# Kernel tuning notes

Hardware: AMD Instinct MI355X
Metric: run time of the kernel (lower is better)

The kernel has to match this reference:

```python
import jax, jax.numpy as jnp
import numpy as np

B, C_IN, C_OUT, D, H, W = 2, 128, 128, 16, 32, 32


def setup_inputs() -> dict:
    key = jax.random.key(0)
    kx, kw, kb = jax.random.split(key, 3)
    x = jax.random.normal(kx, (B, C_IN, D, H, W), dtype=jnp.float32)
    # ddpm_conv3x3 -> Conv3d(in_ch, out_ch, kernel=3, padding=1) with default (scaled-variance) init
    fan_in = C_IN * 3 * 3 * 3
    scale = 1.0 / np.sqrt(fan_in)
    Wk = jax.random.uniform(kw, (C_OUT, C_IN, 3, 3, 3), dtype=jnp.float32, minval=-scale, maxval=scale)
    b = jnp.zeros((C_OUT,), dtype=jnp.float32)
    return {"x": x, "Wk": Wk, "b": b}


def reference(x, Wk, b):
    h = jnp.repeat(jnp.repeat(jnp.repeat(x, 2, axis=2), 2, axis=3), 2, axis=4)
    # 3x3x3 conv, stride 1, padding 1 (SAME)
    out = jax.lax.conv_general_dilated(
        h, Wk,
        window_strides=(1, 1, 1),
        padding="SAME",
        dimension_numbers=("NCDHW", "OIDHW", "NCDHW"),
    )
    return out + b[None, :, None, None, None]
```

## Files before the change

kernel.cpp:

```cpp
#include <hip/hip_runtime.h>
#include <hip/hip_bf16.h>

#define B_    2
#define CIN   128
#define COUT  128
#define DD    16
#define HH    32
#define WW    32
#define OS_H2 64
#define OS_D2 (64*64)
#define OS_CO (32*64*64)
#define OS_B  (COUT*OS_CO)

#define PD_D   18
#define PD_H   34
#define RD     17
#define RDB    68
#define HWDW   (PD_H*RD)
#define PLB    (HWDW*4)
#define CIW    (PD_D*HWDW)
#define CIB    (CIW*4)
#define CI8B   (8*CIB)
#define ARRD   ((size_t)B_*CIN*CIW)
#define ARRB   (ARRD*4)
#define AFOLD_BYTES (8*32*8*64*16)

typedef __attribute__((ext_vector_type(8))) short        short8;
typedef __attribute__((ext_vector_type(4))) float        floatx4;
typedef __attribute__((ext_vector_type(4))) unsigned int uint4v;

static __device__ __forceinline__ unsigned f2bf(float f) {
    union { __hip_bfloat16 h; unsigned short u; } cv;
    cv.h = __float2bfloat16(f);
    return (unsigned)cv.u;
}

__global__ __launch_bounds__(256) void fold_kernel(const float* __restrict__ Wk,
                                                   unsigned short* __restrict__ Afold) {
    const int t = blockIdx.x * 256 + threadIdx.x;
    const int p  = t >> 14;
    const int ks = (t >> 9) & 31;
    const int ct = (t >> 6) & 7;
    const int l  = t & 63;
    const int co = ct * 16 + (l & 15);
    const int ci = ks * 4 + (l >> 4);
    const int ed = (p >> 2) & 1, eh = (p >> 1) & 1, ew = p & 1;

    const float* w = Wk + (co * CIN + ci) * 27;
    float wv[27];
    #pragma unroll
    for (int i = 0; i < 27; ++i) wv[i] = w[i];

    short8 pk;
    #pragma unroll
    for (int tt = 0; tt < 8; ++tt) {
        const int td = (tt >> 2) & 1, th = (tt >> 1) & 1, tw = tt & 1;
        const int dlo = ed ? (td ? 2 : 0) : (td ? 1 : 0);
        const int dhi = ed ? (td ? 2 : 1) : (td ? 2 : 0);
        const int hlo = eh ? (th ? 2 : 0) : (th ? 1 : 0);
        const int hhi = eh ? (th ? 2 : 1) : (th ? 2 : 0);
        const int wlo = ew ? (tw ? 2 : 0) : (tw ? 1 : 0);
        const int whi = ew ? (tw ? 2 : 1) : (tw ? 2 : 0);
        float s = 0.f;
        for (int kd = dlo; kd <= dhi; ++kd)
            for (int kh = hlo; kh <= hhi; ++kh)
                for (int kw = wlo; kw <= whi; ++kw)
                    s += wv[kd * 9 + kh * 3 + kw];
        pk[tt] = (short)f2bf(s);
    }
    reinterpret_cast<short8*>(Afold)[t] = pk;
}

__global__ __launch_bounds__(256) void pad_kernel(const float* __restrict__ x,
                                                  unsigned* __restrict__ xe) {
    const int idx = blockIdx.x * 256 + threadIdx.x;
    const int w2 = idx & 15;
    const int h  = (idx >> 4) & 31;
    const int d  = (idx >> 9) & 15;
    const int ci = (idx >> 13) & 127;
    const int b  = (idx >> 20) & 1;
    const float2 v = *reinterpret_cast<const float2*>(
        x + (size_t)((b * CIN + ci) * DD + d) * (HH * WW) + h * WW + w2 * 2);
    xe[(size_t)((b * CIN + ci) * PD_D + d + 1) * HWDW
       + (h + 1) * RD + (w2 + 1)] = f2bf(v.x) | (f2bf(v.y) << 16);
}

__global__ __launch_bounds__(256) void xo_kernel(const unsigned* __restrict__ xe,
                                                 unsigned* __restrict__ xo) {
    const size_t t = (size_t)blockIdx.x * 256 + threadIdx.x;
    const unsigned e0 = xe[t];
    const unsigned e1 = (t + 1 < ARRD) ? xe[t + 1] : 0u;
    xo[t] = (e0 >> 16) | (e1 << 16);
}

__global__ __launch_bounds__(256, 3) void upconv_mfma(
    const char* __restrict__ xe_c, const char* __restrict__ xo_c,
    const unsigned short* __restrict__ Afold,
    const float* __restrict__ bias,
    float* __restrict__ out)
{
    __shared__ short Bt[2][128 * 64];
    char* buf0 = reinterpret_cast<char*>(&Bt[0][0]);
    char* buf1 = reinterpret_cast<char*>(&Bt[1][0]);

    const int tid  = threadIdx.x;
    const int wave = tid >> 6;
    const int lane = tid & 63;

    const int d      = blockIdx.x >> 3;
    const int h_base = (blockIdx.x & 7) * 4;
    const int p      = blockIdx.y;
    const int b      = blockIdx.z;
    const int ed = (p >> 2) & 1, eh = (p >> 1) & 1, ew = p & 1;

    const int npair = tid & 63;
    const int grp   = tid >> 6;
    const int hl    = npair >> 4;
    const int s     = npair & 15;
    const int n_a   = hl * 32 + 2 * s;
    const int n_b   = n_a + 1;
    const char* pa = ew ? xe_c : xo_c;
    const char* pb = ew ? xo_c : xe_c;
    const int dpad0 = d + ed;
    const int hpad0 = h_base + hl + eh;
    const long rowb = ((long)(b * CIN + grp * 2) * PD_D + dpad0) * (long)PLB
                    + (long)hpad0 * RDB;
    int offA[2], offB[2];
    offA[0] = (int)rowb + (s + ew) * 4;
    offB[0] = (int)rowb + (s + 1) * 4;
    offA[1] = offA[0] + CIB;
    offB[1] = offB[0] + CIB;

    int waddr_a[2], waddr_b[2];
    #pragma unroll
    for (int i = 0; i < 2; ++i) {
        const int cl = grp * 2 + i;
        waddr_a[i] = n_a * 128 + ((cl * 16) ^ (((n_a >> 1) & 7) << 4));
        waddr_b[i] = n_b * 128 + ((cl * 16) ^ (((n_b >> 1) & 7) << 4));
    }

    const int co0 = (wave >> 1) * 64;
    const int n0  = (wave & 1) * 64;
    const int ct0 = (wave >> 1) * 4;
    int raddr[2][4];
    #pragma unroll
    for (int ksl = 0; ksl < 2; ++ksl)
        #pragma unroll
        for (int nt = 0; nt < 4; ++nt) {
            const int n  = n0 + nt * 16 + (lane & 15);
            const int kb = ksl * 64 + (lane >> 4) * 16;
            raddr[ksl][nt] = n * 128 + (kb ^ (((n >> 1) & 7) << 4));
        }

    floatx4 acc[4][4];
    #pragma unroll
    for (int i = 0; i < 4; ++i)
        #pragma unroll
        for (int j = 0; j < 4; ++j)
            acc[i][j] = (floatx4){0.f, 0.f, 0.f, 0.f};

    const short8* Ap = reinterpret_cast<const short8*>(Afold);

    unsigned ga[2][4], gb[2][4];

    #define GATHER()                                                            \
        do {                                                                    \
            _Pragma("unroll")                                                   \
            for (int i = 0; i < 2; ++i) {                                       \
                const char* ba = pa + offA[i];                                  \
                const char* bb = pb + offB[i];                                  \
                ga[i][0] = *(const unsigned*)(ba + 0);                          \
                ga[i][1] = *(const unsigned*)(ba + RDB);                        \
                ga[i][2] = *(const unsigned*)(ba + PLB);                        \
                ga[i][3] = *(const unsigned*)(ba + PLB + RDB);                  \
                gb[i][0] = *(const unsigned*)(bb + 0);                          \
                gb[i][1] = *(const unsigned*)(bb + RDB);                        \
                gb[i][2] = *(const unsigned*)(bb + PLB);                        \
                gb[i][3] = *(const unsigned*)(bb + PLB + RDB);                  \
                offA[i] += CI8B; offB[i] += CI8B;                               \
            }                                                                   \
        } while (0)

    #define BODY(kc, bufc, dofill)                                              \
        do {                                                                    \
            short8 a[2][4];                                                     \
            _Pragma("unroll")                                                   \
            for (int ksl = 0; ksl < 2; ++ksl)                                   \
                _Pragma("unroll")                                               \
                for (int ct = 0; ct < 4; ++ct)                                  \
                    a[ksl][ct] = Ap[(size_t)(((p) * 32 + (kc) * 2 + ksl) * 8    \
                                             + ct0 + ct) * 64 + lane];          \
            _Pragma("unroll")                                                   \
            for (int i = 0; i < 2; ++i) {                                       \
                *(uint4v*)(bufc + waddr_a[i]) =                                 \
                    (uint4v){ga[i][0], ga[i][1], ga[i][2], ga[i][3]};           \
                *(uint4v*)(bufc + waddr_b[i]) =                                 \
                    (uint4v){gb[i][0], gb[i][1], gb[i][2], gb[i][3]};           \
            }                                                                   \
            if (dofill) GATHER();                                               \
            asm volatile("s_waitcnt lgkmcnt(0)\n\ts_barrier" ::: "memory");     \
            __builtin_amdgcn_s_setprio(1);                                      \
            _Pragma("unroll")                                                   \
            for (int ksl = 0; ksl < 2; ++ksl) {                                 \
                short8 bfr[4];                                                  \
                _Pragma("unroll")                                               \
                for (int nt = 0; nt < 4; ++nt)                                  \
                    bfr[nt] = *reinterpret_cast<const short8*>(                 \
                        (bufc) + raddr[ksl][nt]);                               \
                _Pragma("unroll")                                               \
                for (int ct = 0; ct < 4; ++ct)                                  \
                    _Pragma("unroll")                                           \
                    for (int nt = 0; nt < 4; ++nt)                              \
                        acc[ct][nt] = __builtin_amdgcn_mfma_f32_16x16x32_bf16(  \
                            a[ksl][ct], bfr[nt], acc[ct][nt], 0, 0, 0);         \
            }                                                                   \
            __builtin_amdgcn_s_setprio(0);                                      \
        } while (0)

    GATHER();
    for (int kc = 0; kc < 16; kc += 2) {
        BODY(kc,     buf0, true);
        BODY(kc + 1, buf1, (kc + 1) != 15);
    }
    #undef BODY
    #undef GATHER

    float* ob = out + (size_t)b * OS_B + (size_t)(2 * d + ed) * OS_D2;
    #pragma unroll
    for (int ct = 0; ct < 4; ++ct) {
        #pragma unroll
        for (int j = 0; j < 4; ++j) {
            const int co = co0 + ct * 16 + (lane >> 4) * 4 + j;
            const float bv = bias[co];
            #pragma unroll
            for (int nt = 0; nt < 4; ++nt) {
                const int n  = n0 + nt * 16 + (lane & 15);
                const int hh = n >> 5, wl = n & 31;
                const int h2 = 2 * (h_base + hh) + eh;
                const int w2 = 2 * wl + ew;
                ob[(size_t)co * OS_CO + h2 * OS_H2 + w2] = acc[ct][nt][j] + bv;
            }
        }
    }
}

extern "C" void kernel_launch(void* const* d_in, const int* in_sizes, int n_in,
                              void* d_out, int out_size, void* d_ws, size_t ws_size,
                              hipStream_t stream) {
    const float* x    = (const float*)d_in[0];
    const float* Wk   = (const float*)d_in[1];
    const float* bias = (const float*)d_in[2];
    float* out        = (float*)d_out;

    unsigned short* Afold = (unsigned short*)d_ws;
    char* xe = (char*)d_ws + AFOLD_BYTES;
    char* xo = xe + ARRB;

    hipMemsetAsync(xe, 0, ARRB, stream);
    pad_kernel<<<8192, 256, 0, stream>>>(x, (unsigned*)xe);
    xo_kernel<<<(unsigned)(ARRD / 256), 256, 0, stream>>>((const unsigned*)xe,
                                                          (unsigned*)xo);
    fold_kernel<<<512, 256, 0, stream>>>(Wk, Afold);

    dim3 grid(DD * 8, 8, B_);
    upconv_mfma<<<grid, 256, 0, stream>>>(xe, xo, Afold, bias, out);
}
```

Baseline: 115.9 us.

## Vectorize input gather to 16-byte loads, re-layout LDS tile, raise occupancy

The input gather is rebuilt so each thread issues four 16-byte global loads instead of sixteen 4-byte loads. Each thread then writes four LDS chunks in a new ci-major, XOR-swizzled B-tile layout, with matching read addresses for the MFMA fragments. The A-fragment loads move inside the per-k-slice loop to cut live registers, and the launch bound rises from 3 to 4 blocks per CU. The risks are unaligned wide loads (row stride is 68 bytes), new LDS bank-conflict behaviour from the new swizzle, and register spills under the tighter occupancy target.

```diff
diff --git a/kernel.cpp b/kernel.cpp
--- a/kernel.cpp
+++ b/kernel.cpp
@@ -29,10 +29,10 @@
 typedef __attribute__((ext_vector_type(4))) float        floatx4;
 typedef __attribute__((ext_vector_type(4))) unsigned int uint4v;
 
-static __device__ __forceinline__ unsigned f2bf(float f) {
+static __device__ __forceinline__ unsigned short f2bf(float f) {
     union { __hip_bfloat16 h; unsigned short u; } cv;
     cv.h = __float2bfloat16(f);
-    return (unsigned)cv.u;
+    return cv.u;
 }
 
 __global__ __launch_bounds__(256) void fold_kernel(const float* __restrict__ Wk,
@@ -82,7 +82,7 @@
     const float2 v = *reinterpret_cast<const float2*>(
         x + (size_t)((b * CIN + ci) * DD + d) * (HH * WW) + h * WW + w2 * 2);
     xe[(size_t)((b * CIN + ci) * PD_D + d + 1) * HWDW
-       + (h + 1) * RD + (w2 + 1)] = f2bf(v.x) | (f2bf(v.y) << 16);
+       + (h + 1) * RD + (w2 + 1)] = (unsigned)f2bf(v.x) | ((unsigned)f2bf(v.y) << 16);
 }
 
 __global__ __launch_bounds__(256) void xo_kernel(const unsigned* __restrict__ xe,
@@ -93,13 +93,13 @@
     xo[t] = (e0 >> 16) | (e1 << 16);
 }
 
-__global__ __launch_bounds__(256, 3) void upconv_mfma(
+__global__ __launch_bounds__(256, 4) void upconv_mfma(
     const char* __restrict__ xe_c, const char* __restrict__ xo_c,
     const unsigned short* __restrict__ Afold,
     const float* __restrict__ bias,
     float* __restrict__ out)
 {
-    __shared__ short Bt[2][128 * 64];
+    __shared__ short Bt[2][8192];
     char* buf0 = reinterpret_cast<char*>(&Bt[0][0]);
     char* buf1 = reinterpret_cast<char*>(&Bt[1][0]);
 
@@ -113,30 +113,21 @@
     const int b      = blockIdx.z;
     const int ed = (p >> 2) & 1, eh = (p >> 1) & 1, ew = p & 1;
 
-    const int npair = tid & 63;
-    const int grp   = tid >> 6;
-    const int hl    = npair >> 4;
-    const int s     = npair & 15;
-    const int n_a   = hl * 32 + 2 * s;
-    const int n_b   = n_a + 1;
-    const char* pa = ew ? xe_c : xo_c;
-    const char* pb = ew ? xo_c : xe_c;
-    const int dpad0 = d + ed;
-    const int hpad0 = h_base + hl + eh;
-    const long rowb = ((long)(b * CIN + grp * 2) * PD_D + dpad0) * (long)PLB
-                    + (long)hpad0 * RDB;
-    int offA[2], offB[2];
-    offA[0] = (int)rowb + (s + ew) * 4;
-    offB[0] = (int)rowb + (s + 1) * 4;
-    offA[1] = offA[0] + CIB;
-    offB[1] = offB[0] + CIB;
-
-    int waddr_a[2], waddr_b[2];
-    #pragma unroll
-    for (int i = 0; i < 2; ++i) {
-        const int cl = grp * 2 + i;
-        waddr_a[i] = n_a * 128 + ((cl * 16) ^ (((n_a >> 1) & 7) << 4));
-        waddr_b[i] = n_b * 128 + ((cl * 16) ^ (((n_b >> 1) & 7) << 4));
+    const int ci_l  = tid >> 5;
+    const int h_l   = (tid >> 3) & 3;
+    const int phase = (tid >> 2) & 1;
+    const int wg    = tid & 3;
+    const char* pa = phase ? (ew ? xo_c : xe_c) : (ew ? xe_c : xo_c);
+    const int col0 = wg * 4 + (phase ? 1 : ew);
+    const long rowb = ((long)(b * CIN + ci_l) * PD_D + (d + ed)) * (long)PLB
+                    + (long)(h_base + h_l + eh) * RDB;
+    int goff = (int)rowb + col0 * 4;
+
+    int waddr[4];
+    #pragma unroll
+    for (int j = 0; j < 4; ++j) {
+        const int n = h_l * 32 + (wg * 4 + j) * 2 + phase;
+        waddr[j] = ci_l * 2048 + ((n ^ ((n >> 3) & 7)) * 16);
     }
 
     const int co0 = (wave >> 1) * 64;
@@ -147,9 +138,9 @@
     for (int ksl = 0; ksl < 2; ++ksl)
         #pragma unroll
         for (int nt = 0; nt < 4; ++nt) {
+            const int ci = ksl * 4 + (lane >> 4);
             const int n  = n0 + nt * 16 + (lane & 15);
-            const int kb = ksl * 64 + (lane >> 4) * 16;
-            raddr[ksl][nt] = n * 128 + (kb ^ (((n >> 1) & 7) << 4));
+            raddr[ksl][nt] = ci * 2048 + ((n ^ ((n >> 3) & 7)) * 16);
         }
 
     floatx4 acc[4][4];
@@ -161,47 +152,35 @@
 
     const short8* Ap = reinterpret_cast<const short8*>(Afold);
 
-    unsigned ga[2][4], gb[2][4];
+    uint4v g[4];
 
     #define GATHER()                                                            \
         do {                                                                    \
+            const char* bc = pa + goff;                                         \
+            g[0] = *(const uint4v*)(bc);                                        \
+            g[1] = *(const uint4v*)(bc + RDB);                                  \
+            g[2] = *(const uint4v*)(bc + PLB);                                  \
+            g[3] = *(const uint4v*)(bc + PLB + RDB);                            \
+            goff += CI8B;                                                       \
+        } while (0)
+
+    #define BODY(kc, bufc, dofill)                                             \
+        do {                                                                    \
+                                 \
             _Pragma("unroll")                                                   \
-            for (int i = 0; i < 2; ++i) {                                       \
-                const char* ba = pa + offA[i];                                  \
-                const char* bb = pb + offB[i];                                  \
-                ga[i][0] = *(const unsigned*)(ba + 0);                          \
-                ga[i][1] = *(const unsigned*)(ba + RDB);                        \
-                ga[i][2] = *(const unsigned*)(ba + PLB);                        \
-                ga[i][3] = *(const unsigned*)(ba + PLB + RDB);                  \
-                gb[i][0] = *(const unsigned*)(bb + 0);                          \
-                gb[i][1] = *(const unsigned*)(bb + RDB);                        \
-                gb[i][2] = *(const unsigned*)(bb + PLB);                        \
-                gb[i][3] = *(const unsigned*)(bb + PLB + RDB);                  \
-                offA[i] += CI8B; offB[i] += CI8B;                               \
-            }                                                                   \
-        } while (0)
-
-    #define BODY(kc, bufc, dofill)                                              \
-        do {                                                                    \
-            short8 a[2][4];                                                     \
-            _Pragma("unroll")                                                   \
-            for (int ksl = 0; ksl < 2; ++ksl)                                   \
-                _Pragma("unroll")                                               \
-                for (int ct = 0; ct < 4; ++ct)                                  \
-                    a[ksl][ct] = Ap[(size_t)(((p) * 32 + (kc) * 2 + ksl) * 8    \
-                                             + ct0 + ct) * 64 + lane];          \
-            _Pragma("unroll")                                                   \
-            for (int i = 0; i < 2; ++i) {                                       \
-                *(uint4v*)(bufc + waddr_a[i]) =                                 \
-                    (uint4v){ga[i][0], ga[i][1], ga[i][2], ga[i][3]};           \
-                *(uint4v*)(bufc + waddr_b[i]) =                                 \
-                    (uint4v){gb[i][0], gb[i][1], gb[i][2], gb[i][3]};           \
-            }                                                                   \
+            for (int j = 0; j < 4; ++j)                                         \
+                *(uint4v*)((bufc) + waddr[j]) =                                 \
+                    (uint4v){g[0][j], g[1][j], g[2][j], g[3][j]};               \
             if (dofill) GATHER();                                               \
             asm volatile("s_waitcnt lgkmcnt(0)\n\ts_barrier" ::: "memory");     \
             __builtin_amdgcn_s_setprio(1);                                      \
             _Pragma("unroll")                                                   \
             for (int ksl = 0; ksl < 2; ++ksl) {                                 \
+                short8 a[4];                                                    \
+                _Pragma("unroll")                                               \
+                for (int ct = 0; ct < 4; ++ct)                                  \
+                    a[ct] = Ap[(size_t)(((p) * 32 + (kc) * 2 + ksl) * 8         \
+                                        + ct0 + ct) * 64 + lane];               \
                 short8 bfr[4];                                                  \
                 _Pragma("unroll")                                               \
                 for (int nt = 0; nt < 4; ++nt)                                  \
@@ -212,7 +191,7 @@
                     _Pragma("unroll")                                           \
                     for (int nt = 0; nt < 4; ++nt)                              \
                         acc[ct][nt] = __builtin_amdgcn_mfma_f32_16x16x32_bf16(  \
-                            a[ksl][ct], bfr[nt], acc[ct][nt], 0, 0, 0);         \
+                            a[ct], bfr[nt], acc[ct][nt], 0, 0, 0);              \
             }                                                                   \
             __builtin_amdgcn_s_setprio(0);                                      \
         } while (0)
```

Measured after the change: 216.2 us. +86.4%, slower.
